# Optimization experiments

Measured on AMD Instinct MI355X. Metric: run time of the kernel, lower is better.

## Reference

```python
import jax, jax.numpy as jnp
import numpy as np

N_PATCHES = 262144
N_BAGS = 32
INPUT_DIM = 1024
FEAT_DIM = 256
ATTN_DIM = 128
HEAD_DIM = 2


def setup_inputs() -> dict:
    key = jax.random.key(0)
    ks = jax.random.split(key, 9)
    s = 0.02
    return {
        "features": jax.random.normal(ks[0], (N_PATCHES, INPUT_DIM), jnp.float32),
        "W1": jax.random.normal(ks[1], (FEAT_DIM, INPUT_DIM), jnp.float32) * s,
        "b1": jnp.zeros((FEAT_DIM,), jnp.float32),
        "Wa1": jax.random.normal(ks[2], (ATTN_DIM, FEAT_DIM), jnp.float32) * s,
        "ba1": jnp.zeros((ATTN_DIM,), jnp.float32),
        "Wa2": jax.random.normal(ks[3], (1, ATTN_DIM), jnp.float32) * s,
        "ba2": jnp.zeros((1,), jnp.float32),
        "Wh": jax.random.normal(ks[4], (HEAD_DIM, FEAT_DIM), jnp.float32) * s,
        "bh": jnp.zeros((HEAD_DIM,), jnp.float32),
        "bag_sizes": jnp.full((N_BAGS,), N_PATCHES // N_BAGS, jnp.int32),
    }


def reference(features, W1, b1, Wa1, ba1, Wa2, ba2, Wh, bh, bag_sizes):
    # encoder: Linear(input_dim -> features_dim) + ReLU
    h = jax.nn.relu(features @ W1.T + b1)                        # [N, F]
    # attention MLP: Linear -> tanh -> Linear -> scalar score
    a = jnp.tanh(h @ Wa1.T + ba1)                                # [N, A]
    scores = (a @ Wa2.T + ba2)[:, 0]                             # [N]
    # segmented softmax over bags + attention-weighted reduce
    seg = jnp.repeat(jnp.arange(N_BAGS), bag_sizes, total_repeat_length=N_PATCHES)
    m = jax.ops.segment_max(scores, seg, num_segments=N_BAGS)    # [B]
    e = jnp.exp(scores - m[seg])                                 # [N]
    z = jax.ops.segment_sum(e, seg, num_segments=N_BAGS)         # [B]
    attn = e / z[seg]                                            # [N]
    bag_emb = jax.ops.segment_sum(attn[:, None] * h, seg, num_segments=N_BAGS)  # [B, F]
    # linear head
    return bag_emb @ Wh.T + bh                                   # [B, head_dim]
```

## Files before the change

### kernel.cpp

```cpp
#include <hip/hip_runtime.h>
#include <cstdint>
#include <cstddef>

typedef short short8 __attribute__((ext_vector_type(8)));
typedef float f32x4 __attribute__((ext_vector_type(4)));
typedef int   i32x4 __attribute__((ext_vector_type(4)));

#define NPATCH 262144
#define NBAGS  32
#define IN_DIM 1024
#define F_DIM  256
#define A_DIM  128
#define ROWSB  128
#define NBLK   (NPATCH / ROWSB)

__device__ __forceinline__ unsigned short f2bf(float f){
  uint32_t u = __builtin_bit_cast(uint32_t, f);
  u += 0x7fffu + ((u >> 16) & 1u);
  return (unsigned short)(u >> 16);
}
__device__ __forceinline__ float bf2f(unsigned short h){
  return __builtin_bit_cast(float, (uint32_t)h << 16);
}
__device__ __forceinline__ float tanh_fast(float x){
  float e = __expf(2.f * x);
  return (e - 1.f) * __builtin_amdgcn_rcpf(e + 1.f);
}
__device__ __forceinline__ uint32_t cvtpk(float a, float b){
  uint32_t r;
  asm("v_cvt_pk_bf16_f32 %0, %1, %2" : "=v"(r) : "v"(a), "v"(b));
  return r;
}
__device__ __forceinline__ void gload_lds16(const void* g, void* l){
  __builtin_amdgcn_global_load_lds((const __attribute__((address_space(1))) void*)g,
                                   (__attribute__((address_space(3))) void*)l, 16, 0, 0);
}

#define MFMA(a,b,c) __builtin_amdgcn_mfma_f32_16x16x32_bf16((a),(b),(c),0,0,0)
#define SWZH(r) (((r) & 7) << 4)

__global__ void prep_kernel(const float* __restrict__ W1, const float* __restrict__ Wa1,
                            unsigned short* __restrict__ w1b, unsigned short* __restrict__ wa1b,
                            float* __restrict__ bagAcc){
  int id = blockIdx.x * 256 + threadIdx.x;
  if (id < F_DIM*IN_DIM) {
    w1b[id] = f2bf(W1[id]);
  } else if (id < F_DIM*IN_DIM + A_DIM*F_DIM) {
    int j = id - F_DIM*IN_DIM;
    wa1b[j] = f2bf(Wa1[j]);
  } else if (id < F_DIM*IN_DIM + A_DIM*F_DIM + NBAGS*257) {
    bagAcc[id - (F_DIM*IN_DIM + A_DIM*F_DIM)] = 0.f;
  }
}

__global__ __launch_bounds__(256, 2)
void mil_main(const float* __restrict__ feat,
              const unsigned short* __restrict__ w1b,
              const float* __restrict__ b1,
              const unsigned short* __restrict__ wa1b,
              const float* __restrict__ ba1,
              const float* __restrict__ wa2,
              const float* __restrict__ ba2v,
              float* __restrict__ bagAcc)
{
  extern __shared__ char lds[];
  char* Bt0 = lds;
  char* Bt1 = lds + 32768;
  char* HsB = lds;
  float* sc4  = (float*)(lds + 65536);
  float* evec = (float*)(lds + 65536 + 2048);
  float* Pp   = (float*)(lds + 65536 + 2048 + 512);

  const int tid  = threadIdx.x;
  const int wid  = tid >> 6;
  const int lane = tid & 63;
  const int l15  = lane & 15;
  const int l4   = lane >> 4;
  const int bRow = blockIdx.x * ROWSB;
  const int wRow = wid * 32;

  const float* aG0 = feat + (size_t)(bRow + wRow + l15) * IN_DIM + l4*8;
  const float* aG1 = aG0 + (size_t)16 * IN_DIM;

  const char* srcB = (const char*)w1b
      + (size_t)(wid*64 + (lane >> 3)) * 2048
      + (((lane & 7) * 16) ^ (((lane >> 3) & 7) << 4));

#define STAGEB(bb, g) do { \
    _Pragma("unroll") \
    for (int i_ = 0; i_ < 8; ++i_) \
      gload_lds16(srcB + (size_t)i_*16384 + (size_t)(g)*128, \
                  (bb) + wid*8192 + i_*1024); \
  } while(0)

#define LOADA(R, t) do { \
    const float* p0_ = aG0 + (t)*32; \
    const float* p1_ = aG1 + (t)*32; \
    R[0] = *(const float4*)p0_;  R[1] = *(const float4*)(p0_ + 4); \
    R[2] = *(const float4*)p1_;  R[3] = *(const float4*)(p1_ + 4); \
  } while(0)

#define AFRAG2(a0, a1, R) do { \
    const float* v_ = (const float*)(R); \
    i32x4 w0_ = { (int)cvtpk(v_[0],  v_[1]),  (int)cvtpk(v_[2],  v_[3]), \
                  (int)cvtpk(v_[4],  v_[5]),  (int)cvtpk(v_[6],  v_[7]) }; \
    i32x4 w1_ = { (int)cvtpk(v_[8],  v_[9]),  (int)cvtpk(v_[10], v_[11]), \
                  (int)cvtpk(v_[12], v_[13]), (int)cvtpk(v_[14], v_[15]) }; \
    a0 = __builtin_bit_cast(short8, w0_); \
    a1 = __builtin_bit_cast(short8, w1_); \
  } while(0)

  f32x4 acc[2][16];
  #pragma unroll
  for (int i = 0; i < 2; ++i)
    #pragma unroll
    for (int j = 0; j < 16; ++j) acc[i][j] = (f32x4){0.f, 0.f, 0.f, 0.f};

  float4 aR0[4], aR1[4];

  STAGEB(Bt0, 0);
  LOADA(aR0, 0);
  LOADA(aR1, 1);
  asm volatile("s_waitcnt vmcnt(8)" ::: "memory");
  __builtin_amdgcn_sched_barrier(0);
  __builtin_amdgcn_s_barrier();

  const int swzk = (l15 & 7) << 4;
  const int rb   = l15 * 128;

  for (int g = 0; g < 16; ++g){
    const char* bb = (g & 1) ? Bt1 : Bt0;
    char*       bn = (g & 1) ? Bt0 : Bt1;
    if (g < 15) STAGEB(bn, g + 1);
    __builtin_amdgcn_sched_barrier(0);

    #pragma unroll
    for (int s = 0; s < 2; ++s){
      short8 af0, af1;
      if (s == 0){
        AFRAG2(af0, af1, aR0);
        if (g < 15) LOADA(aR0, 2*g + 2);
      } else {
        AFRAG2(af0, af1, aR1);
        if (g < 15) LOADA(aR1, 2*g + 3);
      }
      __builtin_amdgcn_sched_barrier(0);
      const int off = rb + ((s*64 + l4*16) ^ swzk);
      #pragma unroll
      for (int nf = 0; nf < 16; ++nf){
        short8 bf = *(const short8*)(bb + nf*2048 + off);
        acc[0][nf] = MFMA(af0, bf, acc[0][nf]);
        acc[1][nf] = MFMA(af1, bf, acc[1][nf]);
      }
    }
    asm volatile("s_waitcnt vmcnt(8)" ::: "memory");
    __builtin_amdgcn_sched_barrier(0);
    __builtin_amdgcn_s_barrier();
  }
  __syncthreads();

#undef STAGEB
#undef LOADA
#undef AFRAG2

  #pragma unroll
  for (int nf = 0; nf < 16; ++nf){
    float b1v = b1[nf*16 + l15];
    #pragma unroll
    for (int mf = 0; mf < 2; ++mf)
      #pragma unroll
      for (int r = 0; r < 4; ++r){
        int row = wRow + mf*16 + l4*4 + r;
        int col = nf*16 + l15;
        float v = fmaxf(acc[mf][nf][r] + b1v, 0.f);
        int by = (row*512 + col*2) ^ SWZH(row);
        *(unsigned short*)(HsB + by) = f2bf(v);
      }
  }
  __syncthreads();

  f32x4 acc2[8][2];
  #pragma unroll
  for (int i = 0; i < 8; ++i)
    #pragma unroll
    for (int j = 0; j < 2; ++j) acc2[i][j] = (f32x4){0.f, 0.f, 0.f, 0.f};

  #pragma unroll
  for (int ks2 = 0; ks2 < 8; ++ks2){
    short8 hf[8], wf[2];
    #pragma unroll
    for (int mf = 0; mf < 8; ++mf){
      int row = mf*16 + l15;
      int by  = (row*512 + (ks2*32 + l4*8)*2) ^ SWZH(row);
      hf[mf] = *(const short8*)(HsB + by);
    }
    #pragma unroll
    for (int nf = 0; nf < 2; ++nf){
      int col = wid*32 + nf*16 + l15;
      wf[nf] = *(const short8*)(const void*)(wa1b + col*256 + ks2*32 + l4*8);
    }
    #pragma unroll
    for (int mf = 0; mf < 8; ++mf)
      #pragma unroll
      for (int nf = 0; nf < 2; ++nf)
        acc2[mf][nf] = MFMA(hf[mf], wf[nf], acc2[mf][nf]);
  }

  float ba1v[2], wa2v[2];
  #pragma unroll
  for (int nf = 0; nf < 2; ++nf){
    int col = wid*32 + nf*16 + l15;
    ba1v[nf] = ba1[col];
    wa2v[nf] = wa2[col];
  }
  #pragma unroll
  for (int mf = 0; mf < 8; ++mf)
    #pragma unroll
    for (int r = 0; r < 4; ++r){
      float p = tanh_fast(acc2[mf][0][r] + ba1v[0]) * wa2v[0]
              + tanh_fast(acc2[mf][1][r] + ba1v[1]) * wa2v[1];
      p += __shfl_xor(p, 1);
      p += __shfl_xor(p, 2);
      p += __shfl_xor(p, 4);
      p += __shfl_xor(p, 8);
      if (l15 == 0){
        int row = mf*16 + l4*4 + r;
        sc4[row*4 + wid] = p;
      }
    }
  __syncthreads();

  if (tid < 128){
    float s = sc4[tid*4+0] + sc4[tid*4+1] + sc4[tid*4+2] + sc4[tid*4+3] + ba2v[0];
    evec[tid] = __expf(s);
  }
  __syncthreads();

  {
    const int f0 = (tid & 127) << 1;
    const int g  = tid >> 7;
    float p0 = 0.f, p1 = 0.f;
    const int rbase = g << 6;
    #pragma unroll 8
    for (int i = 0; i < 64; ++i){
      const int r = rbase + i;
      const uint32_t hw = *(const uint32_t*)(HsB + ((r*512 + f0*2) ^ SWZH(r)));
      const float e = evec[r];
      p0 = fmaf(e, bf2f((unsigned short)(hw & 0xffffu)), p0);
      p1 = fmaf(e, bf2f((unsigned short)(hw >> 16)),     p1);
    }
    Pp[(g << 8) + f0]     = p0;
    Pp[(g << 8) + f0 + 1] = p1;
  }
  __syncthreads();

  const int bag = bRow >> 13;
  {
    float s = Pp[tid] + Pp[256 + tid];
    atomicAdd(&bagAcc[bag*257 + tid], s);
  }
  if (tid < 64){
    float se = evec[tid] + evec[tid + 64];
    se += __shfl_xor(se, 1);
    se += __shfl_xor(se, 2);
    se += __shfl_xor(se, 4);
    se += __shfl_xor(se, 8);
    se += __shfl_xor(se, 16);
    se += __shfl_xor(se, 32);
    if (tid == 0) atomicAdd(&bagAcc[bag*257 + 256], se);
  }
}

__global__ void head_kernel(const float* __restrict__ bagAcc,
                            const float* __restrict__ wh,
                            const float* __restrict__ bh,
                            float* __restrict__ out){
  int t = threadIdx.x;
  int b = t >> 1, d = t & 1;
  const float* P = bagAcc + b*257;
  float invE = 1.f / P[256];
  float acc = 0.f;
  for (int f = 0; f < 256; ++f) acc += P[f] * wh[d*256 + f];
  out[b*2 + d] = acc * invE + bh[d];
}

extern "C" void kernel_launch(void* const* d_in, const int* in_sizes, int n_in,
                              void* d_out, int out_size, void* d_ws, size_t ws_size,
                              hipStream_t stream){
  const float* feat = (const float*)d_in[0];
  const float* W1   = (const float*)d_in[1];
  const float* b1   = (const float*)d_in[2];
  const float* Wa1  = (const float*)d_in[3];
  const float* ba1  = (const float*)d_in[4];
  const float* Wa2  = (const float*)d_in[5];
  const float* ba2  = (const float*)d_in[6];
  const float* Wh   = (const float*)d_in[7];
  const float* bh   = (const float*)d_in[8];

  unsigned short* w1b  = (unsigned short*)d_ws;
  unsigned short* wa1b = (unsigned short*)((char*)d_ws + 524288);
  float* bagAcc        = (float*)((char*)d_ws + 589824);

  prep_kernel<<<1185, 256, 0, stream>>>(W1, Wa1, w1b, wa1b, bagAcc);

  mil_main<<<NBLK, 256, 70144, stream>>>(feat, w1b, b1, wa1b, ba1,
                                         Wa2, ba2, bagAcc);

  head_kernel<<<1, 64, 0, stream>>>(bagAcc, Wh, bh, (float*)d_out);
}
```

Measured before the change: 289.8 us.

## Split the block across eight waves of sixteen rows each at 512 threads

The main kernel now runs 512 threads per block. Each of the eight waves computes 16 rows instead of 32, so per-thread accumulators and A-fragment registers are halved. The W1 staging, the attention MLP column split, the score reduction and the bag partial sums are all re-partitioned across eight waves, and launch bounds are raised to (512,4) to get more waves resident. In exchange, each B fragment read from LDS now feeds only one MFMA instead of two, doubling LDS traffic per unit of math. The tighter register cap implied by the new launch bounds may also cause spills.

```diff
diff --git a/kernel.cpp b/kernel.cpp
--- a/kernel.cpp
+++ b/kernel.cpp
@@ -53,7 +53,7 @@
   }
 }
 
-__global__ __launch_bounds__(256, 2)
+__global__ __launch_bounds__(512, 4)
 void mil_main(const float* __restrict__ feat,
               const unsigned short* __restrict__ w1b,
               const float* __restrict__ b1,
@@ -67,9 +67,9 @@
   char* Bt0 = lds;
   char* Bt1 = lds + 32768;
   char* HsB = lds;
-  float* sc4  = (float*)(lds + 65536);
-  float* evec = (float*)(lds + 65536 + 2048);
-  float* Pp   = (float*)(lds + 65536 + 2048 + 512);
+  float* sc8  = (float*)(lds + 65536);
+  float* evec = (float*)(lds + 65536 + 4096);
+  float* Pp   = (float*)(lds + 65536 + 4096 + 512);
 
   const int tid  = threadIdx.x;
   const int wid  = tid >> 6;
@@ -77,51 +77,46 @@
   const int l15  = lane & 15;
   const int l4   = lane >> 4;
   const int bRow = blockIdx.x * ROWSB;
-  const int wRow = wid * 32;
-
-  const float* aG0 = feat + (size_t)(bRow + wRow + l15) * IN_DIM + l4*8;
-  const float* aG1 = aG0 + (size_t)16 * IN_DIM;
-
-  const char* srcB = (const char*)w1b
-      + (size_t)(wid*64 + (lane >> 3)) * 2048
-      + (((lane & 7) * 16) ^ (((lane >> 3) & 7) << 4));
+  const int wRow = wid * 16;
+
+  const float* aG = feat + (size_t)(bRow + wRow + l15) * IN_DIM + l4*8;
+
+  const char* srcB;
+  {
+    int D0 = wid*4096 + lane*16;
+    int c0 = D0 >> 7, k0 = D0 & 127;
+    srcB = (const char*)w1b + (size_t)c0*2048 + (k0 ^ ((c0 & 7) << 4));
+  }
 
 #define STAGEB(bb, g) do { \
     _Pragma("unroll") \
-    for (int i_ = 0; i_ < 8; ++i_) \
+    for (int i_ = 0; i_ < 4; ++i_) \
       gload_lds16(srcB + (size_t)i_*16384 + (size_t)(g)*128, \
-                  (bb) + wid*8192 + i_*1024); \
+                  (bb) + wid*4096 + i_*1024); \
   } while(0)
 
 #define LOADA(R, t) do { \
-    const float* p0_ = aG0 + (t)*32; \
-    const float* p1_ = aG1 + (t)*32; \
-    R[0] = *(const float4*)p0_;  R[1] = *(const float4*)(p0_ + 4); \
-    R[2] = *(const float4*)p1_;  R[3] = *(const float4*)(p1_ + 4); \
+    const float* p_ = aG + (t)*32; \
+    R[0] = *(const float4*)p_;  R[1] = *(const float4*)(p_ + 4); \
   } while(0)
 
-#define AFRAG2(a0, a1, R) do { \
+#define AFRAG(af, R) do { \
     const float* v_ = (const float*)(R); \
-    i32x4 w0_ = { (int)cvtpk(v_[0],  v_[1]),  (int)cvtpk(v_[2],  v_[3]), \
-                  (int)cvtpk(v_[4],  v_[5]),  (int)cvtpk(v_[6],  v_[7]) }; \
-    i32x4 w1_ = { (int)cvtpk(v_[8],  v_[9]),  (int)cvtpk(v_[10], v_[11]), \
-                  (int)cvtpk(v_[12], v_[13]), (int)cvtpk(v_[14], v_[15]) }; \
-    a0 = __builtin_bit_cast(short8, w0_); \
-    a1 = __builtin_bit_cast(short8, w1_); \
+    i32x4 w_ = { (int)cvtpk(v_[0], v_[1]), (int)cvtpk(v_[2], v_[3]), \
+                 (int)cvtpk(v_[4], v_[5]), (int)cvtpk(v_[6], v_[7]) }; \
+    af = __builtin_bit_cast(short8, w_); \
   } while(0)
 
-  f32x4 acc[2][16];
+  f32x4 acc[16];
   #pragma unroll
-  for (int i = 0; i < 2; ++i)
-    #pragma unroll
-    for (int j = 0; j < 16; ++j) acc[i][j] = (f32x4){0.f, 0.f, 0.f, 0.f};
-
-  float4 aR0[4], aR1[4];
+  for (int j = 0; j < 16; ++j) acc[j] = (f32x4){0.f, 0.f, 0.f, 0.f};
+
+  float4 aR0[2], aR1[2];
 
   STAGEB(Bt0, 0);
   LOADA(aR0, 0);
   LOADA(aR1, 1);
-  asm volatile("s_waitcnt vmcnt(8)" ::: "memory");
+  asm volatile("s_waitcnt vmcnt(4)" ::: "memory");
   __builtin_amdgcn_sched_barrier(0);
   __builtin_amdgcn_s_barrier();
 
@@ -136,12 +131,12 @@
 
     #pragma unroll
     for (int s = 0; s < 2; ++s){
-      short8 af0, af1;
+      short8 af;
       if (s == 0){
-        AFRAG2(af0, af1, aR0);
+        AFRAG(af, aR0);
         if (g < 15) LOADA(aR0, 2*g + 2);
       } else {
-        AFRAG2(af0, af1, aR1);
+        AFRAG(af, aR1);
         if (g < 15) LOADA(aR1, 2*g + 3);
       }
       __builtin_amdgcn_sched_barrier(0);
@@ -149,11 +144,10 @@
       #pragma unroll
       for (int nf = 0; nf < 16; ++nf){
         short8 bf = *(const short8*)(bb + nf*2048 + off);
-        acc[0][nf] = MFMA(af0, bf, acc[0][nf]);
-        acc[1][nf] = MFMA(af1, bf, acc[1][nf]);
-      }
-    }
-    asm volatile("s_waitcnt vmcnt(8)" ::: "memory");
+        acc[nf] = MFMA(af, bf, acc[nf]);
+      }
+    }
+    asm volatile("s_waitcnt vmcnt(4) lgkmcnt(0)" ::: "memory");
     __builtin_amdgcn_sched_barrier(0);
     __builtin_amdgcn_s_barrier();
   }
@@ -161,77 +155,62 @@
 
 #undef STAGEB
 #undef LOADA
-#undef AFRAG2
+#undef AFRAG
 
   #pragma unroll
   for (int nf = 0; nf < 16; ++nf){
     float b1v = b1[nf*16 + l15];
     #pragma unroll
-    for (int mf = 0; mf < 2; ++mf)
+    for (int r = 0; r < 4; ++r){
+      int row = wRow + l4*4 + r;
+      int col = nf*16 + l15;
+      float v = fmaxf(acc[nf][r] + b1v, 0.f);
+      int by = (row*512 + col*2) ^ SWZH(row);
+      *(unsigned short*)(HsB + by) = f2bf(v);
+    }
+  }
+  __syncthreads();
+
+  {
+    const int acol = wid*16 + l15;
+    f32x4 acc2[8];
+    #pragma unroll
+    for (int i = 0; i < 8; ++i) acc2[i] = (f32x4){0.f, 0.f, 0.f, 0.f};
+
+    #pragma unroll
+    for (int ks2 = 0; ks2 < 8; ++ks2){
+      short8 wf = *(const short8*)(const void*)(wa1b + acol*256 + ks2*32 + l4*8);
+      #pragma unroll
+      for (int mf = 0; mf < 8; ++mf){
+        int row = mf*16 + l15;
+        int by  = (row*512 + (ks2*32 + l4*8)*2) ^ SWZH(row);
+        short8 hf = *(const short8*)(HsB + by);
+        acc2[mf] = MFMA(hf, wf, acc2[mf]);
+      }
+    }
+
+    const float ba1v = ba1[acol];
+    const float wa2v = wa2[acol];
+    #pragma unroll
+    for (int mf = 0; mf < 8; ++mf)
       #pragma unroll
       for (int r = 0; r < 4; ++r){
-        int row = wRow + mf*16 + l4*4 + r;
-        int col = nf*16 + l15;
-        float v = fmaxf(acc[mf][nf][r] + b1v, 0.f);
-        int by = (row*512 + col*2) ^ SWZH(row);
-        *(unsigned short*)(HsB + by) = f2bf(v);
-      }
-  }
-  __syncthreads();
-
-  f32x4 acc2[8][2];
-  #pragma unroll
-  for (int i = 0; i < 8; ++i)
-    #pragma unroll
-    for (int j = 0; j < 2; ++j) acc2[i][j] = (f32x4){0.f, 0.f, 0.f, 0.f};
-
-  #pragma unroll
-  for (int ks2 = 0; ks2 < 8; ++ks2){
-    short8 hf[8], wf[2];
-    #pragma unroll
-    for (int mf = 0; mf < 8; ++mf){
-      int row = mf*16 + l15;
-      int by  = (row*512 + (ks2*32 + l4*8)*2) ^ SWZH(row);
-      hf[mf] = *(const short8*)(HsB + by);
-    }
-    #pragma unroll
-    for (int nf = 0; nf < 2; ++nf){
-      int col = wid*32 + nf*16 + l15;
-      wf[nf] = *(const short8*)(const void*)(wa1b + col*256 + ks2*32 + l4*8);
-    }
-    #pragma unroll
-    for (int mf = 0; mf < 8; ++mf)
-      #pragma unroll
-      for (int nf = 0; nf < 2; ++nf)
-        acc2[mf][nf] = MFMA(hf[mf], wf[nf], acc2[mf][nf]);
-  }
-
-  float ba1v[2], wa2v[2];
-  #pragma unroll
-  for (int nf = 0; nf < 2; ++nf){
-    int col = wid*32 + nf*16 + l15;
-    ba1v[nf] = ba1[col];
-    wa2v[nf] = wa2[col];
-  }
-  #pragma unroll
-  for (int mf = 0; mf < 8; ++mf)
-    #pragma unroll
-    for (int r = 0; r < 4; ++r){
-      float p = tanh_fast(acc2[mf][0][r] + ba1v[0]) * wa2v[0]
-              + tanh_fast(acc2[mf][1][r] + ba1v[1]) * wa2v[1];
-      p += __shfl_xor(p, 1);
-      p += __shfl_xor(p, 2);
-      p += __shfl_xor(p, 4);
-      p += __shfl_xor(p, 8);
-      if (l15 == 0){
-        int row = mf*16 + l4*4 + r;
-        sc4[row*4 + wid] = p;
-      }
-    }
+        float p = tanh_fast(acc2[mf][r] + ba1v) * wa2v;
+        p += __shfl_xor(p, 1);
+        p += __shfl_xor(p, 2);
+        p += __shfl_xor(p, 4);
+        p += __shfl_xor(p, 8);
+        if (l15 == 0){
+          int row = mf*16 + l4*4 + r;
+          sc8[row*8 + wid] = p;
+        }
+      }
+  }
   __syncthreads();
 
   if (tid < 128){
-    float s = sc4[tid*4+0] + sc4[tid*4+1] + sc4[tid*4+2] + sc4[tid*4+3] + ba2v[0];
+    float s = sc8[tid*8+0] + sc8[tid*8+1] + sc8[tid*8+2] + sc8[tid*8+3]
+            + sc8[tid*8+4] + sc8[tid*8+5] + sc8[tid*8+6] + sc8[tid*8+7] + ba2v[0];
     evec[tid] = __expf(s);
   }
   __syncthreads();
@@ -240,9 +219,9 @@
     const int f0 = (tid & 127) << 1;
     const int g  = tid >> 7;
     float p0 = 0.f, p1 = 0.f;
-    const int rbase = g << 6;
+    const int rbase = g << 5;
     #pragma unroll 8
-    for (int i = 0; i < 64; ++i){
+    for (int i = 0; i < 32; ++i){
       const int r = rbase + i;
       const uint32_t hw = *(const uint32_t*)(HsB + ((r*512 + f0*2) ^ SWZH(r)));
       const float e = evec[r];
@@ -255,8 +234,8 @@
   __syncthreads();
 
   const int bag = bRow >> 13;
-  {
-    float s = Pp[tid] + Pp[256 + tid];
+  if (tid < 256){
+    float s = Pp[tid] + Pp[256 + tid] + Pp[512 + tid] + Pp[768 + tid];
     atomicAdd(&bagAcc[bag*257 + tid], s);
   }
   if (tid < 64){
@@ -303,8 +282,9 @@
 
   prep_kernel<<<1185, 256, 0, stream>>>(W1, Wa1, w1b, wa1b, bagAcc);
 
-  mil_main<<<NBLK, 256, 70144, stream>>>(feat, w1b, b1, wa1b, ba1,
-                                         Wa2, ba2, bagAcc);
+  const size_t ldsBytes = 65536 + 4096 + 512 + 4096;
+  mil_main<<<NBLK, 512, ldsBytes, stream>>>(feat, w1b, b1, wa1b, ba1,
+                                            Wa2, ba2, bagAcc);
 
   head_kernel<<<1, 64, 0, stream>>>(bagAcc, Wh, bh, (float*)d_out);
 }
```

Result: no change. 291.9 us (+0.7%).
